# Kernel tuning notes

Hardware: AMD Instinct MI355X
Metric: run time of the kernel (lower is better)

Reference implementation:

```python
import jax, jax.numpy as jnp
import numpy as np
import math

U_CONST = 0.5
FAC_DECAY = math.exp(-1.0 / 100.0)  # tau_fac = 100
DEP_DECAY = math.exp(-1.0 / 200.0)  # tau_dep = 200
BATCH, IN_F, OUT_F = 8192, 4096, 128


def setup_inputs() -> dict:
    key = jax.random.key(0)
    k1, k2 = jax.random.split(key)
    # binary spikes in {0,1} as float32
    pre_spike = jax.random.randint(k1, (BATCH, IN_F), 0, 2).astype(jnp.float32)
    # weight ~ U[0.25, 0.75) per torch.rand(out,in)*0.5 + 0.25
    weight = jax.random.uniform(k2, (OUT_F, IN_F), dtype=jnp.float32) * 0.5 + 0.25
    u = jnp.full((BATCH, IN_F), U_CONST, dtype=jnp.float32)  # facilitation state
    x = jnp.ones((BATCH, IN_F), dtype=jnp.float32)           # depression state
    return {"pre_spike": pre_spike, "weight": weight, "u": u, "x": x}


def reference(pre_spike, weight, u, x):
    # release probability per (batch, in_feature); fold onto pre_spike instead of
    # materializing the (batch, out, in) effective weight (same math).
    release_prob = u * x
    out = jnp.einsum('bi,oi->bo', pre_spike * release_prob, weight)  # [B, out]

    # STP state updates (facilitation then depression; x-update uses NEW u)
    u_fd = u * FAC_DECAY
    u_new = u_fd + U_CONST * (1.0 - u_fd) * pre_spike
    x_new = x * DEP_DECAY + (1.0 - x) * DEP_DECAY * (1.0 - pre_spike * u_new)
    return out, u_new, x_new
```

## Files before the change

kernel.cpp:

```cpp
#include <hip/hip_runtime.h>
#include <hip/hip_bf16.h>
#include <cstdint>

#define BATCH 8192
#define IN_F  4096
#define OUT_F 128
#define KSPLIT 4
#define KSLICE (IN_F / KSPLIT)
#define FD 0.99004983374916811f
#define DD 0.99501247919268232f

typedef __attribute__((ext_vector_type(4))) float f32x4;
typedef __attribute__((ext_vector_type(8))) short bf16x8;

__device__ __forceinline__ unsigned short f2bf(float f){
  union { float f; unsigned u; } v; v.f = f;
  unsigned u = v.u;
  return (unsigned short)((u + 0x7FFFu + ((u >> 16) & 1u)) >> 16);
}

__global__ __launch_bounds__(256) void prep_weight_kernel(const float* __restrict__ w,
                                                          unsigned short* __restrict__ wf){
  const int f  = blockIdx.x * 256 + threadIdx.x;
  const int l  = f & 63;
  const int ct = (f >> 6) & 7;
  const int ks = f >> 9;
  const int row = ct * 16 + (l & 15);
  const int k   = ks * 32 + ((l >> 4) << 3);
  const f32x4* src = reinterpret_cast<const f32x4*>(w + (size_t)row * IN_F + k);
  f32x4 a = src[0], b = src[1];
  union { bf16x8 v; unsigned short s[8]; } o;
  o.s[0]=f2bf(a[0]); o.s[1]=f2bf(a[1]); o.s[2]=f2bf(a[2]); o.s[3]=f2bf(a[3]);
  o.s[4]=f2bf(b[0]); o.s[5]=f2bf(b[1]); o.s[6]=f2bf(b[2]); o.s[7]=f2bf(b[3]);
  *reinterpret_cast<bf16x8*>(wf + (size_t)f * 8) = o.v;
}

template<bool WS>
__global__ __launch_bounds__(256) void stp_fused_kernel(
    const float* __restrict__ pre, const float* __restrict__ uin,
    const float* __restrict__ xin, const float* __restrict__ w,
    const unsigned short* __restrict__ wf,
    float* __restrict__ out, float* __restrict__ un_out, float* __restrict__ xn_out)
{
  __shared__ unsigned char lds[2][16 * 128];

  const int tid = threadIdx.x;
  const int rl  = tid >> 4;
  const int c4  = tid & 15;
  const int rowBase = (blockIdx.x >> 2) * 16;
  const int kslice  = blockIdx.x & 3;
  const int kbase   = kslice * KSLICE;
  const size_t base = (size_t)(rowBase + rl) * IN_F + kbase + (c4 << 2);

  const int l  = tid & 63;
  const int wv = tid >> 6;

  const int wbyte = ((rl * 128) + (c4 << 3)) ^ ((rl & 7) << 4);
  const int arow  = l & 15;
  const int asw   = (arow & 7) << 4;
  const int abase = arow * 128 + ((l >> 4) << 4);

  f32x4 s4 = *reinterpret_cast<const f32x4*>(pre + base);
  f32x4 u4 = *reinterpret_cast<const f32x4*>(uin + base);
  f32x4 x4 = *reinterpret_cast<const f32x4*>(xin + base);

  f32x4 acc0 = {0.f,0.f,0.f,0.f}, acc1 = {0.f,0.f,0.f,0.f};

  for (int ki = 0; ki < KSLICE / 64; ++ki){
    const size_t g = base + (size_t)(ki << 6);

    f32x4 un, xn;
    uint2 pk;
    {
      unsigned short rb[4];
      #pragma unroll
      for (int j = 0; j < 4; ++j){
        const float s = s4[j], u = u4[j], x = x4[j];
        rb[j] = f2bf(u * x * s);
        const float ufd = u * FD;
        const float unj = ufd + 0.5f * (1.0f - ufd) * s;
        un[j] = unj;
        xn[j] = x * DD + (1.0f - x) * DD * (1.0f - s * unj);
      }
      pk.x = (unsigned)rb[0] | ((unsigned)rb[1] << 16);
      pk.y = (unsigned)rb[2] | ((unsigned)rb[3] << 16);
    }
    *reinterpret_cast<f32x4*>(un_out + g) = un;
    *reinterpret_cast<f32x4*>(xn_out + g) = xn;
    *reinterpret_cast<uint2*>(&lds[ki & 1][wbyte]) = pk;

    __syncthreads();

    if (ki < KSLICE / 64 - 1){
      const size_t gn = base + (size_t)((ki + 1) << 6);
      s4 = *reinterpret_cast<const f32x4*>(pre + gn);
      u4 = *reinterpret_cast<const f32x4*>(uin + gn);
      x4 = *reinterpret_cast<const f32x4*>(xin + gn);
    }

    const unsigned char* buf = lds[ki & 1];
    #pragma unroll
    for (int t2 = 0; t2 < 2; ++t2){
      const int ab = (abase + (t2 << 6)) ^ asw;
      bf16x8 af = *reinterpret_cast<const bf16x8*>(buf + ab);
      bf16x8 b0f, b1f;
      const int ks = (kbase >> 5) + (ki << 1) + t2;
      if (WS){
        const bf16x8* wfp = reinterpret_cast<const bf16x8*>(wf);
        b0f = wfp[(size_t)((ks * 8 + 2 * wv)     * 64 + l)];
        b1f = wfp[(size_t)((ks * 8 + 2 * wv + 1) * 64 + l)];
      } else {
        const int kg = ks * 32 + ((l >> 4) << 3);
        const int r0 = (2 * wv) * 16 + (l & 15);
        const f32x4* p0 = reinterpret_cast<const f32x4*>(w + (size_t)r0 * IN_F + kg);
        const f32x4* p1 = reinterpret_cast<const f32x4*>(w + (size_t)(r0 + 16) * IN_F + kg);
        f32x4 a0 = p0[0], a1 = p0[1], c0 = p1[0], c1 = p1[1];
        union { bf16x8 v; unsigned short s[8]; } t;
        t.s[0]=f2bf(a0[0]); t.s[1]=f2bf(a0[1]); t.s[2]=f2bf(a0[2]); t.s[3]=f2bf(a0[3]);
        t.s[4]=f2bf(a1[0]); t.s[5]=f2bf(a1[1]); t.s[6]=f2bf(a1[2]); t.s[7]=f2bf(a1[3]);
        b0f = t.v;
        t.s[0]=f2bf(c0[0]); t.s[1]=f2bf(c0[1]); t.s[2]=f2bf(c0[2]); t.s[3]=f2bf(c0[3]);
        t.s[4]=f2bf(c1[0]); t.s[5]=f2bf(c1[1]); t.s[6]=f2bf(c1[2]); t.s[7]=f2bf(c1[3]);
        b1f = t.v;
      }
      acc0 = __builtin_amdgcn_mfma_f32_16x16x32_bf16(af, b0f, acc0, 0, 0, 0);
      acc1 = __builtin_amdgcn_mfma_f32_16x16x32_bf16(af, b1f, acc1, 0, 0, 0);
    }
  }

  const int colBase = wv * 32 + (l & 15);
  const int rbase   = rowBase + ((l >> 4) << 2);
  #pragma unroll
  for (int rg = 0; rg < 4; ++rg){
    unsafeAtomicAdd(&out[(size_t)(rbase + rg) * OUT_F + colBase],      acc0[rg]);
    unsafeAtomicAdd(&out[(size_t)(rbase + rg) * OUT_F + colBase + 16], acc1[rg]);
  }
}

extern "C" void kernel_launch(void* const* d_in, const int* in_sizes, int n_in,
                              void* d_out, int out_size, void* d_ws, size_t ws_size,
                              hipStream_t stream){
  const float* pre = (const float*)d_in[0];
  const float* w   = (const float*)d_in[1];
  const float* u   = (const float*)d_in[2];
  const float* x   = (const float*)d_in[3];
  float* out    = (float*)d_out;
  float* un_out = out + (size_t)BATCH * OUT_F;
  float* xn_out = un_out + (size_t)BATCH * IN_F;
  unsigned short* wf = (unsigned short*)d_ws;

  hipMemsetAsync(out, 0, (size_t)BATCH * OUT_F * sizeof(float), stream);

  const bool use_ws = (ws_size >= (size_t)(1 << 20));
  const int grid = (BATCH / 16) * KSPLIT;
  if (use_ws){
    prep_weight_kernel<<<256, 256, 0, stream>>>(w, wf);
    stp_fused_kernel<true><<<grid, 256, 0, stream>>>(pre, u, x, w, wf, out, un_out, xn_out);
  } else {
    stp_fused_kernel<false><<<grid, 256, 0, stream>>>(pre, u, x, w, nullptr, out, un_out, xn_out);
  }
}
```

Measured before the change: 174.4 us.

## Have each wave own 16 rows across all output columns, dropping LDS staging

Restructures the fused kernel so every wave computes its own 16 batch rows directly in the MFMA A-fragment layout, loading 8 consecutive k values per lane. This removes the LDS round-trip and __syncthreads, and each wave keeps 8 accumulators covering all 128 output columns. KSPLIT rises to 8 with 64 rows per block, which changes the grid shape and atomic count. Each wave now reads the full weight slice per k-step, raising weight traffic per row tile, and the extra accumulators raise register pressure.

```diff
diff --git a/kernel.cpp b/kernel.cpp
--- a/kernel.cpp
+++ b/kernel.cpp
@@ -5,12 +5,14 @@
 #define BATCH 8192
 #define IN_F  4096
 #define OUT_F 128
-#define KSPLIT 4
+#define KSPLIT 8
 #define KSLICE (IN_F / KSPLIT)
+#define NKS    (KSLICE / 32)
 #define FD 0.99004983374916811f
 #define DD 0.99501247919268232f
 
 typedef __attribute__((ext_vector_type(4))) float f32x4;
+typedef __attribute__((ext_vector_type(8))) float f32x8;
 typedef __attribute__((ext_vector_type(8))) short bf16x8;
 
 __device__ __forceinline__ unsigned short f2bf(float f){
@@ -42,98 +44,81 @@
     const unsigned short* __restrict__ wf,
     float* __restrict__ out, float* __restrict__ un_out, float* __restrict__ xn_out)
 {
-  __shared__ unsigned char lds[2][16 * 128];
+  const int tid = threadIdx.x;
+  const int wv  = tid >> 6;
+  const int l   = tid & 63;
 
-  const int tid = threadIdx.x;
-  const int rl  = tid >> 4;
-  const int c4  = tid & 15;
-  const int rowBase = (blockIdx.x >> 2) * 16;
-  const int kslice  = blockIdx.x & 3;
-  const int kbase   = kslice * KSLICE;
-  const size_t base = (size_t)(rowBase + rl) * IN_F + kbase + (c4 << 2);
+  const int kslice  = blockIdx.x & (KSPLIT - 1);
+  const int rowBase = (blockIdx.x >> 3) * 64 + wv * 16;
+  const int row     = rowBase + (l & 15);
+  const size_t base = (size_t)row * IN_F + kslice * KSLICE + ((l >> 4) << 3);
 
-  const int l  = tid & 63;
-  const int wv = tid >> 6;
+  f32x4 acc[8];
+  #pragma unroll
+  for (int ct = 0; ct < 8; ++ct) acc[ct] = (f32x4){0.f,0.f,0.f,0.f};
 
-  const int wbyte = ((rl * 128) + (c4 << 3)) ^ ((rl & 7) << 4);
-  const int arow  = l & 15;
-  const int asw   = (arow & 7) << 4;
-  const int abase = arow * 128 + ((l >> 4) << 4);
+  f32x8 sC = *reinterpret_cast<const f32x8*>(pre + base);
+  f32x8 uC = *reinterpret_cast<const f32x8*>(uin + base);
+  f32x8 xC = *reinterpret_cast<const f32x8*>(xin + base);
 
-  f32x4 s4 = *reinterpret_cast<const f32x4*>(pre + base);
-  f32x4 u4 = *reinterpret_cast<const f32x4*>(uin + base);
-  f32x4 x4 = *reinterpret_cast<const f32x4*>(xin + base);
+  for (int ks = 0; ks < NKS; ++ks){
+    const size_t g = base + (size_t)(ks << 5);
 
-  f32x4 acc0 = {0.f,0.f,0.f,0.f}, acc1 = {0.f,0.f,0.f,0.f};
-
-  for (int ki = 0; ki < KSLICE / 64; ++ki){
-    const size_t g = base + (size_t)(ki << 6);
-
-    f32x4 un, xn;
-    uint2 pk;
-    {
-      unsigned short rb[4];
-      #pragma unroll
-      for (int j = 0; j < 4; ++j){
-        const float s = s4[j], u = u4[j], x = x4[j];
-        rb[j] = f2bf(u * x * s);
-        const float ufd = u * FD;
-        const float unj = ufd + 0.5f * (1.0f - ufd) * s;
-        un[j] = unj;
-        xn[j] = x * DD + (1.0f - x) * DD * (1.0f - s * unj);
-      }
-      pk.x = (unsigned)rb[0] | ((unsigned)rb[1] << 16);
-      pk.y = (unsigned)rb[2] | ((unsigned)rb[3] << 16);
-    }
-    *reinterpret_cast<f32x4*>(un_out + g) = un;
-    *reinterpret_cast<f32x4*>(xn_out + g) = xn;
-    *reinterpret_cast<uint2*>(&lds[ki & 1][wbyte]) = pk;
-
-    __syncthreads();
-
-    if (ki < KSLICE / 64 - 1){
-      const size_t gn = base + (size_t)((ki + 1) << 6);
-      s4 = *reinterpret_cast<const f32x4*>(pre + gn);
-      u4 = *reinterpret_cast<const f32x4*>(uin + gn);
-      x4 = *reinterpret_cast<const f32x4*>(xin + gn);
+    f32x8 sN, uN, xN;
+    if (ks + 1 < NKS){
+      const size_t gn = base + (size_t)((ks + 1) << 5);
+      sN = *reinterpret_cast<const f32x8*>(pre + gn);
+      uN = *reinterpret_cast<const f32x8*>(uin + gn);
+      xN = *reinterpret_cast<const f32x8*>(xin + gn);
     }
 
-    const unsigned char* buf = lds[ki & 1];
+    f32x8 un, xn;
+    union { bf16x8 v; unsigned short s[8]; } af;
     #pragma unroll
-    for (int t2 = 0; t2 < 2; ++t2){
-      const int ab = (abase + (t2 << 6)) ^ asw;
-      bf16x8 af = *reinterpret_cast<const bf16x8*>(buf + ab);
-      bf16x8 b0f, b1f;
-      const int ks = (kbase >> 5) + (ki << 1) + t2;
-      if (WS){
-        const bf16x8* wfp = reinterpret_cast<const bf16x8*>(wf);
-        b0f = wfp[(size_t)((ks * 8 + 2 * wv)     * 64 + l)];
-        b1f = wfp[(size_t)((ks * 8 + 2 * wv + 1) * 64 + l)];
-      } else {
-        const int kg = ks * 32 + ((l >> 4) << 3);
-        const int r0 = (2 * wv) * 16 + (l & 15);
-        const f32x4* p0 = reinterpret_cast<const f32x4*>(w + (size_t)r0 * IN_F + kg);
-        const f32x4* p1 = reinterpret_cast<const f32x4*>(w + (size_t)(r0 + 16) * IN_F + kg);
-        f32x4 a0 = p0[0], a1 = p0[1], c0 = p1[0], c1 = p1[1];
+    for (int j = 0; j < 8; ++j){
+      const float s = sC[j], u = uC[j], x = xC[j];
+      af.s[j] = f2bf(u * x * s);
+      const float ufd = u * FD;
+      const float unj = ufd + 0.5f * (1.0f - ufd) * s;
+      un[j] = unj;
+      xn[j] = x * DD + (1.0f - x) * DD * (1.0f - s * unj);
+    }
+    *reinterpret_cast<f32x8*>(un_out + g) = un;
+    *reinterpret_cast<f32x8*>(xn_out + g) = xn;
+
+    const int gks = kslice * NKS + ks;
+    if (WS){
+      const bf16x8* wfp = reinterpret_cast<const bf16x8*>(wf);
+      #pragma unroll
+      for (int ct = 0; ct < 8; ++ct){
+        bf16x8 bf = wfp[(size_t)((gks * 8 + ct) << 6) + l];
+        acc[ct] = __builtin_amdgcn_mfma_f32_16x16x32_bf16(af.v, bf, acc[ct], 0, 0, 0);
+      }
+    } else {
+      const int kg = gks * 32 + ((l >> 4) << 3);
+      #pragma unroll
+      for (int ct = 0; ct < 8; ++ct){
+        const int r0 = ct * 16 + (l & 15);
+        const f32x4* p = reinterpret_cast<const f32x4*>(w + (size_t)r0 * IN_F + kg);
+        f32x4 a = p[0], b = p[1];
         union { bf16x8 v; unsigned short s[8]; } t;
-        t.s[0]=f2bf(a0[0]); t.s[1]=f2bf(a0[1]); t.s[2]=f2bf(a0[2]); t.s[3]=f2bf(a0[3]);
-        t.s[4]=f2bf(a1[0]); t.s[5]=f2bf(a1[1]); t.s[6]=f2bf(a1[2]); t.s[7]=f2bf(a1[3]);
-        b0f = t.v;
-        t.s[0]=f2bf(c0[0]); t.s[1]=f2bf(c0[1]); t.s[2]=f2bf(c0[2]); t.s[3]=f2bf(c0[3]);
-        t.s[4]=f2bf(c1[0]); t.s[5]=f2bf(c1[1]); t.s[6]=f2bf(c1[2]); t.s[7]=f2bf(c1[3]);
-        b1f = t.v;
+        t.s[0]=f2bf(a[0]); t.s[1]=f2bf(a[1]); t.s[2]=f2bf(a[2]); t.s[3]=f2bf(a[3]);
+        t.s[4]=f2bf(b[0]); t.s[5]=f2bf(b[1]); t.s[6]=f2bf(b[2]); t.s[7]=f2bf(b[3]);
+        acc[ct] = __builtin_amdgcn_mfma_f32_16x16x32_bf16(af.v, t.v, acc[ct], 0, 0, 0);
       }
-      acc0 = __builtin_amdgcn_mfma_f32_16x16x32_bf16(af, b0f, acc0, 0, 0, 0);
-      acc1 = __builtin_amdgcn_mfma_f32_16x16x32_bf16(af, b1f, acc1, 0, 0, 0);
     }
+
+    sC = sN; uC = uN; xC = xN;
   }
 
-  const int colBase = wv * 32 + (l & 15);
-  const int rbase   = rowBase + ((l >> 4) << 2);
+  const int col0 = l & 15;
+  const int r0   = rowBase + ((l >> 4) << 2);
   #pragma unroll
-  for (int rg = 0; rg < 4; ++rg){
-    unsafeAtomicAdd(&out[(size_t)(rbase + rg) * OUT_F + colBase],      acc0[rg]);
-    unsafeAtomicAdd(&out[(size_t)(rbase + rg) * OUT_F + colBase + 16], acc1[rg]);
+  for (int ct = 0; ct < 8; ++ct){
+    #pragma unroll
+    for (int rg = 0; rg < 4; ++rg){
+      unsafeAtomicAdd(&out[(size_t)(r0 + rg) * OUT_F + ct * 16 + col0], acc[ct][rg]);
+    }
   }
 }
 
@@ -152,7 +137,7 @@
   hipMemsetAsync(out, 0, (size_t)BATCH * OUT_F * sizeof(float), stream);
 
   const bool use_ws = (ws_size >= (size_t)(1 << 20));
-  const int grid = (BATCH / 16) * KSPLIT;
+  const int grid = (BATCH / 64) * KSPLIT;
   if (use_ws){
     prep_weight_kernel<<<256, 256, 0, stream>>>(w, wf);
     stp_fused_kernel<true><<<grid, 256, 0, stream>>>(pre, u, x, w, wf, out, un_out, xn_out);
```

Result: slower. 205.5 us (+17.8%).

## Process 256-wide K chunks per sync with 8-wide loads and register prefetch

Applied to the files above, without the earlier changes.

Restructures the fused STP+GEMM loop so each iteration covers a 256-element K chunk instead of 64. Each thread loads 8 floats per row for two rows, and the next chunk is prefetched into registers before the elementwise work. This cuts the number of barriers per block by four and widens memory transactions. It also adds a min-blocks occupancy hint. The cost is more registers and a larger LDS buffer, which may limit occupancy.

```diff
diff --git a/kernel.cpp b/kernel.cpp
--- a/kernel.cpp
+++ b/kernel.cpp
@@ -6,11 +6,14 @@
 #define IN_F  4096
 #define OUT_F 128
 #define KSPLIT 4
-#define KSLICE (IN_F / KSPLIT)
+#define KSL    (IN_F / KSPLIT)
+#define CH     256
+#define NCHUNK (KSL / CH)
 #define FD 0.99004983374916811f
 #define DD 0.99501247919268232f
 
 typedef __attribute__((ext_vector_type(4))) float f32x4;
+typedef __attribute__((ext_vector_type(8))) float f32x8;
 typedef __attribute__((ext_vector_type(8))) short bf16x8;
 
 __device__ __forceinline__ unsigned short f2bf(float f){
@@ -35,105 +38,125 @@
   *reinterpret_cast<bf16x8*>(wf + (size_t)f * 8) = o.v;
 }
 
+__device__ __forceinline__ uint4 stp_ew(const f32x8 s8, const f32x8 u8, const f32x8 x8,
+                                        float* __restrict__ un_p, float* __restrict__ xn_p){
+  f32x8 un, xn;
+  unsigned short rb[8];
+  #pragma unroll
+  for (int j = 0; j < 8; ++j){
+    const float s = s8[j], u = u8[j], x = x8[j];
+    rb[j] = f2bf(u * x * s);
+    const float ufd = u * FD;
+    const float unj = ufd + 0.5f * (1.0f - ufd) * s;
+    un[j] = unj;
+    xn[j] = x * DD + (1.0f - x) * DD * (1.0f - s * unj);
+  }
+  *reinterpret_cast<f32x8*>(un_p) = un;
+  *reinterpret_cast<f32x8*>(xn_p) = xn;
+  uint4 pk;
+  pk.x = (unsigned)rb[0] | ((unsigned)rb[1] << 16);
+  pk.y = (unsigned)rb[2] | ((unsigned)rb[3] << 16);
+  pk.z = (unsigned)rb[4] | ((unsigned)rb[5] << 16);
+  pk.w = (unsigned)rb[6] | ((unsigned)rb[7] << 16);
+  return pk;
+}
+
 template<bool WS>
-__global__ __launch_bounds__(256) void stp_fused_kernel(
+__global__ __launch_bounds__(256, 4) void stp_fused4(
     const float* __restrict__ pre, const float* __restrict__ uin,
     const float* __restrict__ xin, const float* __restrict__ w,
     const unsigned short* __restrict__ wf,
     float* __restrict__ out, float* __restrict__ un_out, float* __restrict__ xn_out)
 {
-  __shared__ unsigned char lds[2][16 * 128];
+  __shared__ unsigned char rbuf[2][16 * CH * 2];
 
   const int tid = threadIdx.x;
-  const int rl  = tid >> 4;
-  const int c4  = tid & 15;
+  const int wv  = tid >> 6;
+  const int l   = tid & 63;
+  const int ksl     = blockIdx.x & (KSPLIT - 1);
   const int rowBase = (blockIdx.x >> 2) * 16;
-  const int kslice  = blockIdx.x & 3;
-  const int kbase   = kslice * KSLICE;
-  const size_t base = (size_t)(rowBase + rl) * IN_F + kbase + (c4 << 2);
+  const int k0      = ksl * KSL;
 
-  const int l  = tid & 63;
-  const int wv = tid >> 6;
+  const int rl0 = 4 * wv + (l >> 5);
+  const size_t g0 = (size_t)(rowBase + rl0) * IN_F + k0 + (size_t)(l & 31) * 8;
+  const size_t rowStride2 = (size_t)2 * IN_F;
 
-  const int wbyte = ((rl * 128) + (c4 << 3)) ^ ((rl & 7) << 4);
-  const int arow  = l & 15;
-  const int asw   = (arow & 7) << 4;
-  const int abase = arow * 128 + ((l >> 4) << 4);
+  const int wb0 = ((rl0    ) * 512 + (l & 31) * 16) ^ (((rl0    ) & 7) << 4);
+  const int wb1 = ((rl0 + 2) * 512 + (l & 31) * 16) ^ (((rl0 + 2) & 7) << 4);
 
-  f32x4 s4 = *reinterpret_cast<const f32x4*>(pre + base);
-  f32x4 u4 = *reinterpret_cast<const f32x4*>(uin + base);
-  f32x4 x4 = *reinterpret_cast<const f32x4*>(xin + base);
+  const int ar  = l & 15;
+  const int akc = (l >> 4) * 16;
 
   f32x4 acc0 = {0.f,0.f,0.f,0.f}, acc1 = {0.f,0.f,0.f,0.f};
 
-  for (int ki = 0; ki < KSLICE / 64; ++ki){
-    const size_t g = base + (size_t)(ki << 6);
+  f32x8 sA0 = *reinterpret_cast<const f32x8*>(pre + g0);
+  f32x8 sA1 = *reinterpret_cast<const f32x8*>(pre + g0 + rowStride2);
+  f32x8 uA0 = *reinterpret_cast<const f32x8*>(uin + g0);
+  f32x8 uA1 = *reinterpret_cast<const f32x8*>(uin + g0 + rowStride2);
+  f32x8 xA0 = *reinterpret_cast<const f32x8*>(xin + g0);
+  f32x8 xA1 = *reinterpret_cast<const f32x8*>(xin + g0 + rowStride2);
 
-    f32x4 un, xn;
-    uint2 pk;
-    {
-      unsigned short rb[4];
-      #pragma unroll
-      for (int j = 0; j < 4; ++j){
-        const float s = s4[j], u = u4[j], x = x4[j];
-        rb[j] = f2bf(u * x * s);
-        const float ufd = u * FD;
-        const float unj = ufd + 0.5f * (1.0f - ufd) * s;
-        un[j] = unj;
-        xn[j] = x * DD + (1.0f - x) * DD * (1.0f - s * unj);
-      }
-      pk.x = (unsigned)rb[0] | ((unsigned)rb[1] << 16);
-      pk.y = (unsigned)rb[2] | ((unsigned)rb[3] << 16);
+  for (int c = 0; c < NCHUNK; ++c){
+    const size_t gc = g0 + (size_t)c * CH;
+
+    f32x8 sB0, sB1, uB0, uB1, xB0, xB1;
+    if (c + 1 < NCHUNK){
+      const size_t gn = g0 + (size_t)(c + 1) * CH;
+      sB0 = *reinterpret_cast<const f32x8*>(pre + gn);
+      sB1 = *reinterpret_cast<const f32x8*>(pre + gn + rowStride2);
+      uB0 = *reinterpret_cast<const f32x8*>(uin + gn);
+      uB1 = *reinterpret_cast<const f32x8*>(uin + gn + rowStride2);
+      xB0 = *reinterpret_cast<const f32x8*>(xin + gn);
+      xB1 = *reinterpret_cast<const f32x8*>(xin + gn + rowStride2);
     }
-    *reinterpret_cast<f32x4*>(un_out + g) = un;
-    *reinterpret_cast<f32x4*>(xn_out + g) = xn;
-    *reinterpret_cast<uint2*>(&lds[ki & 1][wbyte]) = pk;
+
+    uint4 p0 = stp_ew(sA0, uA0, xA0, un_out + gc, xn_out + gc);
+    uint4 p1 = stp_ew(sA1, uA1, xA1, un_out + gc + rowStride2, xn_out + gc + rowStride2);
+    *reinterpret_cast<uint4*>(&rbuf[c & 1][wb0]) = p0;
+    *reinterpret_cast<uint4*>(&rbuf[c & 1][wb1]) = p1;
 
     __syncthreads();
 
-    if (ki < KSLICE / 64 - 1){
-      const size_t gn = base + (size_t)((ki + 1) << 6);
-      s4 = *reinterpret_cast<const f32x4*>(pre + gn);
-      u4 = *reinterpret_cast<const f32x4*>(uin + gn);
-      x4 = *reinterpret_cast<const f32x4*>(xin + gn);
-    }
-
-    const unsigned char* buf = lds[ki & 1];
+    const unsigned char* buf = rbuf[c & 1];
     #pragma unroll
-    for (int t2 = 0; t2 < 2; ++t2){
-      const int ab = (abase + (t2 << 6)) ^ asw;
-      bf16x8 af = *reinterpret_cast<const bf16x8*>(buf + ab);
-      bf16x8 b0f, b1f;
-      const int ks = (kbase >> 5) + (ki << 1) + t2;
+    for (int ks = 0; ks < 8; ++ks){
+      const int rb = (ar * 512 + ks * 64 + akc) ^ ((ar & 7) << 4);
+      bf16x8 af = *reinterpret_cast<const bf16x8*>(buf + rb);
+      const int gks = (k0 >> 5) + c * 8 + ks;
+      bf16x8 b0, b1;
       if (WS){
         const bf16x8* wfp = reinterpret_cast<const bf16x8*>(wf);
-        b0f = wfp[(size_t)((ks * 8 + 2 * wv)     * 64 + l)];
-        b1f = wfp[(size_t)((ks * 8 + 2 * wv + 1) * 64 + l)];
+        b0 = wfp[(size_t)((gks * 8 + 2 * wv    ) << 6) + l];
+        b1 = wfp[(size_t)((gks * 8 + 2 * wv + 1) << 6) + l];
       } else {
-        const int kg = ks * 32 + ((l >> 4) << 3);
+        const int kg = gks * 32 + ((l >> 4) << 3);
         const int r0 = (2 * wv) * 16 + (l & 15);
-        const f32x4* p0 = reinterpret_cast<const f32x4*>(w + (size_t)r0 * IN_F + kg);
-        const f32x4* p1 = reinterpret_cast<const f32x4*>(w + (size_t)(r0 + 16) * IN_F + kg);
-        f32x4 a0 = p0[0], a1 = p0[1], c0 = p1[0], c1 = p1[1];
+        const f32x4* q0 = reinterpret_cast<const f32x4*>(w + (size_t)r0 * IN_F + kg);
+        const f32x4* q1 = reinterpret_cast<const f32x4*>(w + (size_t)(r0 + 16) * IN_F + kg);
+        f32x4 a0 = q0[0], a1 = q0[1], c0 = q1[0], c1 = q1[1];
         union { bf16x8 v; unsigned short s[8]; } t;
         t.s[0]=f2bf(a0[0]); t.s[1]=f2bf(a0[1]); t.s[2]=f2bf(a0[2]); t.s[3]=f2bf(a0[3]);
         t.s[4]=f2bf(a1[0]); t.s[5]=f2bf(a1[1]); t.s[6]=f2bf(a1[2]); t.s[7]=f2bf(a1[3]);
-        b0f = t.v;
+        b0 = t.v;
         t.s[0]=f2bf(c0[0]); t.s[1]=f2bf(c0[1]); t.s[2]=f2bf(c0[2]); t.s[3]=f2bf(c0[3]);
         t.s[4]=f2bf(c1[0]); t.s[5]=f2bf(c1[1]); t.s[6]=f2bf(c1[2]); t.s[7]=f2bf(c1[3]);
-        b1f = t.v;
+        b1 = t.v;
       }
-      acc0 = __builtin_amdgcn_mfma_f32_16x16x32_bf16(af, b0f, acc0, 0, 0, 0);
-      acc1 = __builtin_amdgcn_mfma_f32_16x16x32_bf16(af, b1f, acc1, 0, 0, 0);
+      acc0 = __builtin_amdgcn_mfma_f32_16x16x32_bf16(af, b0, acc0, 0, 0, 0);
+      acc1 = __builtin_amdgcn_mfma_f32_16x16x32_bf16(af, b1, acc1, 0, 0, 0);
+    }
+
+    if (c + 1 < NCHUNK){
+      sA0 = sB0; sA1 = sB1; uA0 = uB0; uA1 = uB1; xA0 = xB0; xA1 = xB1;
     }
   }
 
   const int colBase = wv * 32 + (l & 15);
-  const int rbase   = rowBase + ((l >> 4) << 2);
+  const int r0      = rowBase + ((l >> 4) << 2);
   #pragma unroll
   for (int rg = 0; rg < 4; ++rg){
-    unsafeAtomicAdd(&out[(size_t)(rbase + rg) * OUT_F + colBase],      acc0[rg]);
-    unsafeAtomicAdd(&out[(size_t)(rbase + rg) * OUT_F + colBase + 16], acc1[rg]);
+    unsafeAtomicAdd(&out[(size_t)(r0 + rg) * OUT_F + colBase],      acc0[rg]);
+    unsafeAtomicAdd(&out[(size_t)(r0 + rg) * OUT_F + colBase + 16], acc1[rg]);
   }
 }
 
@@ -155,8 +178,8 @@
   const int grid = (BATCH / 16) * KSPLIT;
   if (use_ws){
     prep_weight_kernel<<<256, 256, 0, stream>>>(w, wf);
-    stp_fused_kernel<true><<<grid, 256, 0, stream>>>(pre, u, x, w, wf, out, un_out, xn_out);
+    stp_fused4<true><<<grid, 256, 0, stream>>>(pre, u, x, w, wf, out, un_out, xn_out);
   } else {
-    stp_fused_kernel<false><<<grid, 256, 0, stream>>>(pre, u, x, w, nullptr, out, un_out, xn_out);
+    stp_fused4<false><<<grid, 256, 0, stream>>>(pre, u, x, w, nullptr, out, un_out, xn_out);
   }
 }
```

After: 167.5 us (median of 2 runs). 1.04x faster.
